# Kernel optimization log

Measured on AMD Instinct MI355X. Metric: run time of the kernel, lower is better.

The kernel has to match this reference:

```python
import jax, jax.numpy as jnp
import numpy as np

B, S, MD, H = 8, 1024, 1024, 16
D = MD // H  # 64
# Faithful to torch: scale = (dim_per_head // num_heads) ** -0.5 (a quirk, not 1/sqrt(D))
SCALE = float((D // H) ** (-0.5))


def setup_inputs() -> dict:
    k0 = jax.random.key(0)
    ks = jax.random.split(k0, 11)
    w = 1.0 / np.sqrt(MD)
    mk = lambda k, shape, s: jax.random.normal(k, shape, dtype=jnp.float32) * s
    return {
        "query": mk(ks[0], (B, S, MD), 1.0),
        "key": mk(ks[1], (B, S, MD), 1.0),
        "value": mk(ks[2], (B, S, MD), 1.0),
        "Wq": mk(ks[3], (MD, MD), w), "bq": mk(ks[4], (MD,), w),
        "Wk": mk(ks[5], (MD, MD), w), "bk": mk(ks[6], (MD,), w),
        "Wv": mk(ks[7], (MD, MD), w), "bv": mk(ks[8], (MD,), w),
        "Wo": mk(ks[9], (MD, MD), w), "bo": mk(ks[10], (MD,), w),
    }


def reference(query, key, value, Wq, bq, Wk, bk, Wv, bv, Wo, bo):
    # Dropout is identity in eval mode (deterministic reference).
    Bq, T, _ = query.shape
    Sk = key.shape[1]
    q = query @ Wq + bq   # [B, T, H*D]
    k = key @ Wk + bk     # [B, S, H*D]
    v = value @ Wv + bv
    # Faithful replication of torch .view(B*H, -1, D): plain row-major reshape
    # (NOT a head transpose -- it chunks sequence/head indices together).
    q = q.reshape(Bq * H, T, D)
    k = k.reshape(Bq * H, Sk, D)
    v = v.reshape(Bq * H, Sk, D)
    attn = jnp.einsum('btd,bsd->bts', q, k) * SCALE          # [B*H, T, S]
    p = jax.nn.softmax(attn, axis=-1)
    ctx = jnp.einsum('bts,bsd->btd', p, v).reshape(Bq, T, H * D)
    output = ctx @ Wo + bo                                    # [B, T, MD]
    a = attn.reshape(Bq, H, T, Sk)
    attn_post = jax.nn.sigmoid(a).sum(axis=1) / H             # [B, T, S]
    return output, attn_post
```

## Files before the change

kernel.cpp:

```cpp
#include <hip/hip_runtime.h>


typedef __attribute__((ext_vector_type(8))) short bf16x8;
typedef __attribute__((ext_vector_type(4))) float f32x4;

static __device__ __forceinline__ short f2bf(float f) {
  union { float f; unsigned u; } v; v.f = f;
  unsigned lsb = (v.u >> 16) & 1u;
  v.u += 0x7fffu + lsb;
  return (short)(v.u >> 16);
}

static __device__ __forceinline__ short f2bf_rhu(float f) {
  union { float f; unsigned u; } v; v.f = f;
  v.u += 0x8000u;
  return (short)(v.u >> 16);
}

static __device__ __forceinline__ float exp2_hw(float x) {
  float r;
  asm("v_exp_f32 %0, %1" : "=v"(r) : "v"(x));
  return r;
}

#define L2E_HALF 0.72134752f

#define GLDS16(gp, lp) __builtin_amdgcn_global_load_lds( \
    (const __attribute__((address_space(1))) void*)(gp), \
    (__attribute__((address_space(3))) void*)(lp), 16, 0, 0)

struct Ptr4 { const float* s[4]; short* d[4]; };
struct Ptr3 { const float* s[3]; short* d[3]; };
struct QkvArgs { const short* A[3]; const short* B[3]; const float* bias[3]; short* C[3]; };

__global__ __launch_bounds__(256) void convt4(Ptr4 a)
{
  const float* __restrict__ src = a.s[blockIdx.z];
  short* __restrict__ dst = a.d[blockIdx.z];
  __shared__ float T[64][65];
  const int tid = threadIdx.x;
  const int c0 = blockIdx.x * 64, r0 = blockIdx.y * 64;
  {
    const int rr = tid >> 4, cc = (tid & 15) * 4;
    for (int i = 0; i < 4; ++i) {
      int row = rr + i * 16;
      const float4 v = *(const float4*)(src + (size_t)(r0 + row) * 1024 + c0 + cc);
      T[row][cc] = v.x; T[row][cc + 1] = v.y; T[row][cc + 2] = v.z; T[row][cc + 3] = v.w;
    }
  }
  __syncthreads();
  {
    const int rr = tid >> 3, cc = (tid & 7) * 8;
    for (int i = 0; i < 2; ++i) {
      int row = rr + i * 32;
      bf16x8 v;
      for (int j = 0; j < 8; ++j) v[j] = f2bf(T[cc + j][row]);
      *(bf16x8*)(dst + (size_t)(c0 + row) * 1024 + r0 + cc) = v;
    }
  }
}

__global__ __launch_bounds__(256) void cvt3(Ptr3 a)
{
  const float* __restrict__ src = a.s[blockIdx.z];
  short* __restrict__ dst = a.d[blockIdx.z];
  const size_t i = ((size_t)blockIdx.x * 256 + threadIdx.x) * 8;
  const float4 v0 = *(const float4*)(src + i);
  const float4 v1 = *(const float4*)(src + i + 4);
  bf16x8 o;
  o[0] = f2bf(v0.x); o[1] = f2bf(v0.y); o[2] = f2bf(v0.z); o[3] = f2bf(v0.w);
  o[4] = f2bf(v1.x); o[5] = f2bf(v1.y); o[6] = f2bf(v1.z); o[7] = f2bf(v1.w);
  *(bf16x8*)(dst + i) = o;
}

__global__ __launch_bounds__(256) void transp_v(
    const short* __restrict__ src, short* __restrict__ dst)
{
  __shared__ short T[64][72];
  const int g = blockIdx.y, t0 = blockIdx.x * 64;
  const short* s = src + (size_t)g * 65536 + (size_t)t0 * 64;
  short* d = dst + (size_t)g * 65536 + t0;
  const int r = threadIdx.x >> 3, c = (threadIdx.x & 7) * 8;
  for (int i = 0; i < 2; ++i) {
    bf16x8 v = *(const bf16x8*)(s + (size_t)(r + i * 32) * 64 + c);
    *(bf16x8*)(&T[r + i * 32][c]) = v;
  }
  __syncthreads();
  for (int i = 0; i < 2; ++i) {
    int dr = r + i * 32;
    bf16x8 v;
    for (int j = 0; j < 8; ++j) v[j] = T[c + j][dr];
    *(bf16x8*)(d + (size_t)dr * 1024 + c) = v;
  }
}

static __device__ __forceinline__ void gemm_body(
    const short* __restrict__ A, const short* __restrict__ BT,
    const float* __restrict__ bias, void* __restrict__ Cp, int mode)
{
  __shared__ short As[2][128 * 64];
  __shared__ short Bs[2][128 * 64];
  const int K = 1024, N = 1024;
  const int tid = threadIdx.x;
  const int lane = tid & 63, wave = tid >> 6;
  const int quad = lane >> 4, l16 = lane & 15;
  const int wm = (wave & 1) * 64, wn = (wave >> 1) * 64;
  const int lin = blockIdx.y * 64 + blockIdx.x;
  const int xcd = lin & 7, idx = lin >> 3;
  const int bx = xcd * 8 + (idx & 7);
  const int by = idx >> 3;
  const int bm = bx * 128, bn = by * 128;

  f32x4 acc[4][4] = {};

  const int s_row = tid >> 3;
  const int s_col = (tid & 7) * 8;
  const int lds_base = wave * 512;

  for (int i = 0; i < 4; ++i) {
    int row = s_row + i * 32;
    GLDS16(A + (size_t)(bm + row) * K + s_col, &As[0][i * 2048 + lds_base]);
    GLDS16(BT + (size_t)(bn + row) * K + s_col, &Bs[0][i * 2048 + lds_base]);
  }
  __syncthreads();

  int cur = 0;
  for (int t = 0; t < 16; ++t) {
    if (t < 15) {
      const int k0 = (t + 1) * 64;
      for (int i = 0; i < 4; ++i) {
        int row = s_row + i * 32;
        GLDS16(A + (size_t)(bm + row) * K + k0 + s_col, &As[cur ^ 1][i * 2048 + lds_base]);
        GLDS16(BT + (size_t)(bn + row) * K + k0 + s_col, &Bs[cur ^ 1][i * 2048 + lds_base]);
      }
    }
    for (int ks = 0; ks < 2; ++ks) {
      bf16x8 af[4], bfr[4];
      for (int mi = 0; mi < 4; ++mi)
        af[mi] = *(const bf16x8*)(&As[cur][(wm + mi * 16 + l16) * 64 + ks * 32 + quad * 8]);
      for (int ni = 0; ni < 4; ++ni)
        bfr[ni] = *(const bf16x8*)(&Bs[cur][(wn + ni * 16 + l16) * 64 + ks * 32 + quad * 8]);
      for (int mi = 0; mi < 4; ++mi)
        for (int ni = 0; ni < 4; ++ni)
          acc[mi][ni] = __builtin_amdgcn_mfma_f32_16x16x32_bf16(af[mi], bfr[ni], acc[mi][ni], 0, 0, 0);
    }
    __syncthreads();
    cur ^= 1;
  }

  for (int ni = 0; ni < 4; ++ni) {
    int col = bn + wn + ni * 16 + l16;
    float bv = bias[col];
    for (int mi = 0; mi < 4; ++mi) {
      int row0 = bm + wm + mi * 16 + quad * 4;
      for (int r = 0; r < 4; ++r) {
        int row = row0 + r;
        float fv = acc[mi][ni][r] + bv;
        if (mode == 2) ((float*)Cp)[(size_t)row * N + col] = fv;
        else           ((short*)Cp)[(size_t)row * N + col] = f2bf(fv);
      }
    }
  }
}

__global__ __launch_bounds__(256) void gemm_bt16(
    const short* __restrict__ A, const short* __restrict__ BT,
    const float* __restrict__ bias, void* __restrict__ Cp, int mode)
{
  gemm_body(A, BT, bias, Cp, mode);
}

__global__ __launch_bounds__(256) void gemm_qkv(QkvArgs a)
{
  const int z = blockIdx.z;
  gemm_body(a.A[z], a.B[z], a.bias[z], a.C[z], 0);
}

__global__ __launch_bounds__(256, 1) void attn_fused8(
    const short* __restrict__ Qp, const short* __restrict__ Kp,
    const short* __restrict__ VpT,
    short* __restrict__ ctx,
    float* __restrict__ attn_post)
{
  __shared__ short Plds[32][1032];
  __shared__ float red[32][4];

  const int tid = threadIdx.x;
  const int wave = tid >> 6, lane = tid & 63;
  const int quad = lane >> 4, l16 = lane & 15;
  const int orig = blockIdx.x;
  const int b = orig & 7;
  const int t0 = (orig >> 3) * 32;
  const int sbase = wave * 256;

  float sig[2][16][4] = {};

  for (int h = 0; h < 16; ++h) {
    const int g = b * 16 + h;
    const short* Qg = Qp + (size_t)g * 65536;
    const short* Kg = Kp + (size_t)g * 65536;
    const short* Vg = VpT + (size_t)g * 65536;

    bf16x8 aq[2][2];
#pragma unroll
    for (int tt = 0; tt < 2; ++tt) {
      aq[tt][0] = *(const bf16x8*)(Qg + (t0 + tt * 16 + l16) * 64 + quad * 8);
      aq[tt][1] = *(const bf16x8*)(Qg + (t0 + tt * 16 + l16) * 64 + 32 + quad * 8);
    }

    float rsum[2][4] = {};

    bf16x8 kb0[4], kb1[4];
#pragma unroll
    for (int t = 0; t < 4; ++t) {
      int s = sbase + t * 16;
      kb0[t] = *(const bf16x8*)(Kg + (s + l16) * 64 + quad * 8);
      kb1[t] = *(const bf16x8*)(Kg + (s + l16) * 64 + 32 + quad * 8);
    }
#pragma unroll
    for (int tile = 0; tile < 16; ++tile) {
      const int slot = tile & 3;
      bf16x8 bk0 = kb0[slot], bk1 = kb1[slot];
      if (tile < 12) {
        int s = sbase + (tile + 4) * 16;
        kb0[slot] = *(const bf16x8*)(Kg + (s + l16) * 64 + quad * 8);
        kb1[slot] = *(const bf16x8*)(Kg + (s + l16) * 64 + 32 + quad * 8);
      }
#pragma unroll
      for (int tt = 0; tt < 2; ++tt) {
        f32x4 c = {0.f, 0.f, 0.f, 0.f};
        c = __builtin_amdgcn_mfma_f32_16x16x32_bf16(aq[tt][0], bk0, c, 0, 0, 0);
        c = __builtin_amdgcn_mfma_f32_16x16x32_bf16(aq[tt][1], bk1, c, 0, 0, 0);
#pragma unroll
        for (int r = 0; r < 4; ++r) {
          float e = exp2_hw(c[r] * L2E_HALF);
          rsum[tt][r] += e;
          Plds[tt * 16 + quad * 4 + r][sbase + tile * 16 + l16] = f2bf_rhu(e);
          sig[tt][tile][r] += e * __builtin_amdgcn_rcpf(1.f + e);
        }
      }
    }
#pragma unroll
    for (int tt = 0; tt < 2; ++tt)
      for (int r = 0; r < 4; ++r)
        for (int mask = 1; mask < 16; mask <<= 1)
          rsum[tt][r] += __shfl_xor(rsum[tt][r], mask, 64);
    if (l16 == 0)
#pragma unroll
      for (int tt = 0; tt < 2; ++tt)
        for (int r = 0; r < 4; ++r)
          red[tt * 16 + quad * 4 + r][wave] = rsum[tt][r];
    __syncthreads();

    const short* Vw = Vg + (size_t)(wave * 16 + l16) * 1024;
    f32x4 acc[2][2] = {};
#pragma unroll
    for (int sl = 0; sl < 32; ++sl) {
      bf16x8 v  = *(const bf16x8*)(Vw + sl * 32 + quad * 8);
      bf16x8 p0 = *(const bf16x8*)(&Plds[l16][sl * 32 + quad * 8]);
      bf16x8 p1 = *(const bf16x8*)(&Plds[16 + l16][sl * 32 + quad * 8]);
      acc[0][sl & 1] = __builtin_amdgcn_mfma_f32_16x16x32_bf16(p0, v, acc[0][sl & 1], 0, 0, 0);
      acc[1][sl & 1] = __builtin_amdgcn_mfma_f32_16x16x32_bf16(p1, v, acc[1][sl & 1], 0, 0, 0);
    }

    short* ctxg = ctx + (size_t)g * 65536 + t0 * 64;
#pragma unroll
    for (int tt = 0; tt < 2; ++tt)
      for (int r = 0; r < 4; ++r) {
        int row = tt * 16 + quad * 4 + r;
        float s4 = red[row][0] + red[row][1] + red[row][2] + red[row][3];
        float inv = __builtin_amdgcn_rcpf(s4);
        float cval = (acc[tt][0][r] + acc[tt][1][r]) * inv;
        ctxg[row * 64 + wave * 16 + l16] = f2bf(cval);
      }
    __syncthreads();
  }

  float* ap_out = attn_post + (size_t)b * 1048576 + (size_t)t0 * 1024;
#pragma unroll
  for (int tt = 0; tt < 2; ++tt)
    for (int tile = 0; tile < 16; ++tile)
      for (int r = 0; r < 4; ++r)
        ap_out[(tt * 16 + quad * 4 + r) * 1024 + sbase + tile * 16 + l16] =
            sig[tt][tile][r] * 0.0625f;
}

extern "C" void kernel_launch(void* const* d_in, const int* in_sizes, int n_in,
                              void* d_out, int out_size, void* d_ws, size_t ws_size,
                              hipStream_t stream) {
  const float* query = (const float*)d_in[0];
  const float* key   = (const float*)d_in[1];
  const float* value = (const float*)d_in[2];
  const float* Wq = (const float*)d_in[3]; const float* bq = (const float*)d_in[4];
  const float* Wk = (const float*)d_in[5]; const float* bk = (const float*)d_in[6];
  const float* Wv = (const float*)d_in[7]; const float* bv = (const float*)d_in[8];
  const float* Wo = (const float*)d_in[9]; const float* bo = (const float*)d_in[10];

  float* out0 = (float*)d_out;
  float* attn_post = out0 + (8u << 20);

  short* WqT = (short*)d_ws;
  short* WkT = WqT + (1u << 20);
  short* WvT = WkT + (1u << 20);
  short* WoT = WvT + (1u << 20);
  short* Qp  = WoT + (1u << 20);
  short* Kp  = Qp + (8u << 20);
  short* VpT = Kp + (8u << 20);

  dim3 blk(256);
  dim3 ggrid(64, 8);
  const size_t NEED_BIG = (size_t)(60u << 20) * 2;

  convt4<<<dim3(16, 16, 4), blk, 0, stream>>>(
      Ptr4{{Wq, Wk, Wv, Wo}, {WqT, WkT, WvT, WoT}});

  short* ctx;
  if (ws_size >= NEED_BIG) {
    short* Xq = VpT + (8u << 20);
    short* Xk = Xq + (8u << 20);
    short* Xv = Xk + (8u << 20);
    short* Vflat = Xv + (8u << 20);
    ctx = Xq;

    cvt3<<<dim3(4096, 1, 3), blk, 0, stream>>>(Ptr3{{query, key, value}, {Xq, Xk, Xv}});
    gemm_qkv<<<dim3(64, 8, 3), blk, 0, stream>>>(
        QkvArgs{{Xq, Xk, Xv}, {WqT, WkT, WvT}, {bq, bk, bv}, {Qp, Kp, Vflat}});
    transp_v<<<dim3(16, 128), blk, 0, stream>>>(Vflat, VpT);
  } else {
    short* Xin = VpT + (8u << 20);
    short* Vflat = Xin + (8u << 20);
    ctx = Xin;

    cvt3<<<dim3(4096, 1, 1), blk, 0, stream>>>(Ptr3{{query, query, query}, {Xin, Xin, Xin}});
    gemm_bt16<<<ggrid, blk, 0, stream>>>(Xin, WqT, bq, Qp, 0);
    cvt3<<<dim3(4096, 1, 1), blk, 0, stream>>>(Ptr3{{key, key, key}, {Xin, Xin, Xin}});
    gemm_bt16<<<ggrid, blk, 0, stream>>>(Xin, WkT, bk, Kp, 0);
    cvt3<<<dim3(4096, 1, 1), blk, 0, stream>>>(Ptr3{{value, value, value}, {Xin, Xin, Xin}});
    gemm_bt16<<<ggrid, blk, 0, stream>>>(Xin, WvT, bv, Vflat, 0);
    transp_v<<<dim3(16, 128), blk, 0, stream>>>(Vflat, VpT);
  }

  attn_fused8<<<dim3(256), blk, 0, stream>>>(Qp, Kp, VpT, ctx, attn_post);
  gemm_bt16<<<ggrid, blk, 0, stream>>>(ctx, WoT, bo, out0, 2);
}
```

Baseline: 455.6 us.

## Split attention heads across two blocks and combine sigmoid partials

Each attention block now processes half of the 16 heads, which doubles the grid from 256 to 512 blocks and allows two blocks per CU through launch bounds. The second half-head block writes its sigmoid partial sum as bf16 into a workspace buffer, and a new add_post kernel adds that buffer into attn_post. This targets low occupancy on a GPU with many CUs, where 256 blocks underfill the device. In exchange it adds an extra launch plus roughly 16MB write and 48MB read-modify traffic, and bf16 rounding of half the sigmoid sum costs some precision. Two blocks per CU may also increase register pressure for the large sig array.

```diff
diff --git a/kernel.cpp b/kernel.cpp
--- a/kernel.cpp
+++ b/kernel.cpp
@@ -9,6 +9,12 @@
   unsigned lsb = (v.u >> 16) & 1u;
   v.u += 0x7fffu + lsb;
   return (short)(v.u >> 16);
+}
+
+static __device__ __forceinline__ float bf2f(short s) {
+  union { float f; unsigned u; } v;
+  v.u = ((unsigned)(unsigned short)s) << 16;
+  return v.f;
 }
 
 static __device__ __forceinline__ short f2bf_rhu(float f) {
@@ -71,6 +77,19 @@
   o[0] = f2bf(v0.x); o[1] = f2bf(v0.y); o[2] = f2bf(v0.z); o[3] = f2bf(v0.w);
   o[4] = f2bf(v1.x); o[5] = f2bf(v1.y); o[6] = f2bf(v1.z); o[7] = f2bf(v1.w);
   *(bf16x8*)(dst + i) = o;
+}
+
+__global__ __launch_bounds__(256) void add_post(
+    float* __restrict__ ap, const short* __restrict__ part)
+{
+  const size_t i = ((size_t)blockIdx.x * 256 + threadIdx.x) * 8;
+  float4 a0 = *(float4*)(ap + i);
+  float4 a1 = *(float4*)(ap + i + 4);
+  const bf16x8 p = *(const bf16x8*)(part + i);
+  a0.x += bf2f(p[0]); a0.y += bf2f(p[1]); a0.z += bf2f(p[2]); a0.w += bf2f(p[3]);
+  a1.x += bf2f(p[4]); a1.y += bf2f(p[5]); a1.z += bf2f(p[6]); a1.w += bf2f(p[7]);
+  *(float4*)(ap + i) = a0;
+  *(float4*)(ap + i + 4) = a1;
 }
 
 __global__ __launch_bounds__(256) void transp_v(
@@ -176,11 +195,12 @@
   gemm_body(a.A[z], a.B[z], a.bias[z], a.C[z], 0);
 }
 
-__global__ __launch_bounds__(256, 1) void attn_fused8(
+__global__ __launch_bounds__(256, 2) void attn_fused11(
     const short* __restrict__ Qp, const short* __restrict__ Kp,
     const short* __restrict__ VpT,
     short* __restrict__ ctx,
-    float* __restrict__ attn_post)
+    float* __restrict__ attn_post,
+    short* __restrict__ part)
 {
   __shared__ short Plds[32][1032];
   __shared__ float red[32][4];
@@ -190,12 +210,13 @@
   const int quad = lane >> 4, l16 = lane & 15;
   const int orig = blockIdx.x;
   const int b = orig & 7;
-  const int t0 = (orig >> 3) * 32;
+  const int hg = (orig >> 3) & 1;
+  const int t0 = (orig >> 4) * 32;
   const int sbase = wave * 256;
 
   float sig[2][16][4] = {};
 
-  for (int h = 0; h < 16; ++h) {
+  for (int h = hg * 8; h < hg * 8 + 8; ++h) {
     const int g = b * 16 + h;
     const short* Qg = Qp + (size_t)g * 65536;
     const short* Kg = Kp + (size_t)g * 65536;
@@ -276,13 +297,23 @@
     __syncthreads();
   }
 
-  float* ap_out = attn_post + (size_t)b * 1048576 + (size_t)t0 * 1024;
-#pragma unroll
-  for (int tt = 0; tt < 2; ++tt)
-    for (int tile = 0; tile < 16; ++tile)
-      for (int r = 0; r < 4; ++r)
-        ap_out[(tt * 16 + quad * 4 + r) * 1024 + sbase + tile * 16 + l16] =
-            sig[tt][tile][r] * 0.0625f;
+  if (hg == 0) {
+    float* ap_out = attn_post + (size_t)b * 1048576 + (size_t)t0 * 1024;
+#pragma unroll
+    for (int tt = 0; tt < 2; ++tt)
+      for (int tile = 0; tile < 16; ++tile)
+        for (int r = 0; r < 4; ++r)
+          ap_out[(tt * 16 + quad * 4 + r) * 1024 + sbase + tile * 16 + l16] =
+              sig[tt][tile][r] * 0.0625f;
+  } else {
+    short* pp = part + (size_t)b * 1048576 + (size_t)t0 * 1024;
+#pragma unroll
+    for (int tt = 0; tt < 2; ++tt)
+      for (int tile = 0; tile < 16; ++tile)
+        for (int r = 0; r < 4; ++r)
+          pp[(tt * 16 + quad * 4 + r) * 1024 + sbase + tile * 16 + l16] =
+              f2bf(sig[tt][tile][r] * 0.0625f);
+  }
 }
 
 extern "C" void kernel_launch(void* const* d_in, const int* in_sizes, int n_in,
@@ -315,12 +346,14 @@
       Ptr4{{Wq, Wk, Wv, Wo}, {WqT, WkT, WvT, WoT}});
 
   short* ctx;
+  short* part;
   if (ws_size >= NEED_BIG) {
     short* Xq = VpT + (8u << 20);
     short* Xk = Xq + (8u << 20);
     short* Xv = Xk + (8u << 20);
     short* Vflat = Xv + (8u << 20);
     ctx = Xq;
+    part = Vflat;
 
     cvt3<<<dim3(4096, 1, 3), blk, 0, stream>>>(Ptr3{{query, key, value}, {Xq, Xk, Xv}});
     gemm_qkv<<<dim3(64, 8, 3), blk, 0, stream>>>(
@@ -330,6 +363,7 @@
     short* Xin = VpT + (8u << 20);
     short* Vflat = Xin + (8u << 20);
     ctx = Xin;
+    part = Vflat;
 
     cvt3<<<dim3(4096, 1, 1), blk, 0, stream>>>(Ptr3{{query, query, query}, {Xin, Xin, Xin}});
     gemm_bt16<<<ggrid, blk, 0, stream>>>(Xin, WqT, bq, Qp, 0);
@@ -340,6 +374,7 @@
     transp_v<<<dim3(16, 128), blk, 0, stream>>>(Vflat, VpT);
   }
 
-  attn_fused8<<<dim3(256), blk, 0, stream>>>(Qp, Kp, VpT, ctx, attn_post);
+  attn_fused11<<<dim3(512), blk, 0, stream>>>(Qp, Kp, VpT, ctx, attn_post, part);
+  add_post<<<dim3(4096), blk, 0, stream>>>(attn_post, part);
   gemm_bt16<<<ggrid, blk, 0, stream>>>(ctx, WoT, bo, out0, 2);
 }
```

New measurement: 527.5 us. 15.8% more time.
